# Performance work log

Measured on AMD Instinct MI355X. Metric: run time of the kernel, lower is better.

## Reference

```python
import jax, jax.numpy as jnp
import numpy as np
import math

N_HEAD = 8
D_MODEL = 512
HEAD_SIZE = D_MODEL // N_HEAD
VOCAB = 16384
BLOCK = 512
LN_EPS = 1e-5


def sinusoidal_pe(max_len, dim):
    pos = np.arange(max_len)[:, None].astype(np.float32)
    div = np.exp(np.arange(0, dim, 2).astype(np.float32) * (-math.log(10000.0) / dim))
    pe = np.zeros((max_len, dim), dtype=np.float32)
    pe[:, 0::2] = np.sin(pos * div)
    pe[:, 1::2] = np.cos(pos * div)
    return jnp.asarray(pe)  # (max_len, hs)


def setup_inputs() -> dict:
    key = jax.random.key(0)
    ks = jax.random.split(key, 6)
    b, t = 4, BLOCK
    return {
        "x": jax.random.normal(ks[0], (b, t, 1), dtype=jnp.float32),
        "embedding": jax.random.normal(ks[1], (N_HEAD, VOCAB, HEAD_SIZE), dtype=jnp.float32),
        "enc_w": jax.random.normal(ks[2], (D_MODEL, 1), dtype=jnp.float32) * 0.05,
        "enc_b": jax.random.normal(ks[3], (D_MODEL,), dtype=jnp.float32) * 0.05,
        "ln_w": jnp.ones((HEAD_SIZE,), dtype=jnp.float32),
        "ln_b": jnp.zeros((HEAD_SIZE,), dtype=jnp.float32),
        "dec_w": jax.random.normal(ks[4], (1, D_MODEL), dtype=jnp.float32) * 0.05,
        "dec_b": jax.random.normal(ks[5], (1,), dtype=jnp.float32) * 0.05,
    }


def reference(x, embedding, enc_w, enc_b, ln_w, ln_b, dec_w, dec_b):
    b, t, _ = x.shape
    # encoder: Linear(input_dim -> d_model)
    h = x @ enc_w.T + enc_b                              # (b, t, d_model)
    h = h.reshape(b, t, N_HEAD, HEAD_SIZE).transpose(0, 2, 1, 3)  # (b, nh, t, hs)
    # sinusoidal positional encoding over time, added to head dim
    h = h + sinusoidal_pe(BLOCK, HEAD_SIZE)[:t]
    # LayerNorm over hs
    mu = h.mean(-1, keepdims=True)
    var = ((h - mu) ** 2).mean(-1, keepdims=True)
    h = (h - mu) * jax.lax.rsqrt(var + LN_EPS) * ln_w + ln_b
    # attention over shared per-head codebook
    scores = jnp.einsum('bnth,nvh->bntv', h, embedding) / math.sqrt(D_MODEL)
    probs = jax.nn.softmax(scores, axis=-1)              # (b, nh, t, vocab)
    quant = jnp.einsum('bntv,nvh->bnth', probs, embedding)
    quant = quant.transpose(0, 2, 1, 3).reshape(b, t, D_MODEL)
    # decoder: Linear(d_model -> output_dim)
    return quant @ dec_w.T + dec_b                       # (b, t, 1)
```

## Files before the change

### kernel.cpp

```cpp
#include <hip/hip_runtime.h>
#include <hip/hip_bf16.h>
#include <math.h>

#define NH 8
#define HS 64
#define VOCAB 16384
#define QPH 2048
#define NSLICE 32
#define QSCALE (0.04419417382415922f * 1.4426950408889634f)

typedef __attribute__((ext_vector_type(8))) short bf16x8;
typedef __attribute__((ext_vector_type(4))) float f32x4;

static __device__ __forceinline__ unsigned short f2bf(float f) {
    __hip_bfloat16 h = __float2bfloat16(f);
    unsigned short u;
    __builtin_memcpy(&u, &h, 2);
    return u;
}

static __device__ __forceinline__ float fexp2(float x) {
#if __has_builtin(__builtin_amdgcn_exp2f)
    return __builtin_amdgcn_exp2f(x);
#else
    return __expf(x * 0.6931471805599453f);
#endif
}

__global__ void eprep(const float* __restrict__ emb, const float* __restrict__ dec_w,
                      unsigned short* __restrict__ ebf, float* __restrict__ g) {
    int i4  = blockIdx.x * 256 + threadIdx.x;
    int row = i4 >> 4;
    int c   = i4 & 15;
    int n   = row >> 14;
    f32x4 v = ((const f32x4*)emb)[i4];
    ushort4 u = make_ushort4(f2bf(v.x), f2bf(v.y), f2bf(v.z), f2bf(v.w));
    ((ushort4*)ebf)[i4] = u;
    const float* dw = dec_w + n * 64 + c * 4;
    float p = v.x * dw[0] + v.y * dw[1] + v.z * dw[2] + v.w * dw[3];
    p += __shfl_xor(p, 1); p += __shfl_xor(p, 2);
    p += __shfl_xor(p, 4); p += __shfl_xor(p, 8);
    if (c == 0) g[row] = p;
}

__global__ void qprep(const float* __restrict__ x, const float* __restrict__ enc_w,
                      const float* __restrict__ enc_b, const float* __restrict__ ln_w,
                      const float* __restrict__ ln_b, unsigned short* __restrict__ qbf) {
    int row  = blockIdx.x * 4 + (threadIdx.x >> 6);
    int h    = threadIdx.x & 63;
    int n = row >> 11;
    int q = row & 2047;
    int t = q & 511;
    float xv = x[q];
    int d = n * 64 + h;
    float h2  = (float)(h & ~1);
    float div = __expf(h2 * (-9.210340371976184f / 64.0f));
    float ang = (float)t * div;
    float pe  = (h & 1) ? __cosf(ang) : __sinf(ang);
    float v = xv * enc_w[d] + enc_b[d] + pe;
    float s = v;
    #pragma unroll
    for (int off = 1; off < 64; off <<= 1) s += __shfl_xor(s, off);
    float mu = s * (1.0f / 64.0f);
    float dd = v - mu;
    float s2 = dd * dd;
    #pragma unroll
    for (int off = 1; off < 64; off <<= 1) s2 += __shfl_xor(s2, off);
    float var = s2 * (1.0f / 64.0f);
    float y = dd * rsqrtf(var + 1e-5f) * ln_w[h] + ln_b[h];
    qbf[row * 64 + h] = f2bf(y * QSCALE);
}

__global__ void __launch_bounds__(256, 3)
attn(const unsigned short* __restrict__ qbf, const unsigned short* __restrict__ ebf,
     const float* __restrict__ g, float2* __restrict__ part) {
    int tid  = threadIdx.x;
    int w    = tid >> 6;
    int lane = tid & 63;
    int quad = lane >> 4;
    int l15  = lane & 15;
    int head   = blockIdx.x & 7;
    int vslice = (blockIdx.x >> 3) & 31;
    int qchunk = blockIdx.x >> 8;
    int qbase  = (qchunk * 4 + w) * 128;

    const short* qp = (const short*)qbf + (size_t)(head * QPH + qbase) * HS;
    bf16x8 qf[8][2];
    #pragma unroll
    for (int qt = 0; qt < 8; ++qt) {
        const short* qrow = qp + (qt * 16 + l15) * HS + quad * 8;
        qf[qt][0] = *(const bf16x8*)(qrow);
        qf[qt][1] = *(const bf16x8*)(qrow + 32);
    }

    const short* ep = (const short*)ebf + ((size_t)head * VOCAB + vslice * 512) * HS;
    const float* gp = g + head * VOCAB + vslice * 512;

    float num[8] = {0.f, 0.f, 0.f, 0.f, 0.f, 0.f, 0.f, 0.f};
    float den[8] = {0.f, 0.f, 0.f, 0.f, 0.f, 0.f, 0.f, 0.f};
    const f32x4 z = {0.f, 0.f, 0.f, 0.f};

    #pragma clang loop unroll(disable)
    for (int it = 0; it < 16; ++it) {
        int vb = it * 32;
        const short* e0 = ep + (size_t)(vb + l15) * HS + quad * 8;
        const short* e1 = ep + (size_t)(vb + 16 + l15) * HS + quad * 8;
        bf16x8 a00 = *(const bf16x8*)(e0);
        bf16x8 a01 = *(const bf16x8*)(e0 + 32);
        bf16x8 a10 = *(const bf16x8*)(e1);
        bf16x8 a11 = *(const bf16x8*)(e1 + 32);
        f32x4 gv0 = *(const f32x4*)(gp + vb + quad * 4);
        f32x4 gv1 = *(const f32x4*)(gp + vb + 16 + quad * 4);
        #pragma unroll
        for (int qt = 0; qt < 8; ++qt) {
            f32x4 acc0 = __builtin_amdgcn_mfma_f32_16x16x32_bf16(a00, qf[qt][0], z, 0, 0, 0);
            acc0       = __builtin_amdgcn_mfma_f32_16x16x32_bf16(a01, qf[qt][1], acc0, 0, 0, 0);
            f32x4 acc1 = __builtin_amdgcn_mfma_f32_16x16x32_bf16(a10, qf[qt][0], z, 0, 0, 0);
            acc1       = __builtin_amdgcn_mfma_f32_16x16x32_bf16(a11, qf[qt][1], acc1, 0, 0, 0);
            #pragma unroll
            for (int r = 0; r < 4; ++r) {
                float p0 = fexp2(acc0[r]);
                float p1 = fexp2(acc1[r]);
                den[qt] += p0 + p1;
                num[qt] += p0 * gv0[r] + p1 * gv1[r];
            }
        }
    }

    #pragma unroll
    for (int qt = 0; qt < 8; ++qt) {
        num[qt] += __shfl_xor(num[qt], 16); num[qt] += __shfl_xor(num[qt], 32);
        den[qt] += __shfl_xor(den[qt], 16); den[qt] += __shfl_xor(den[qt], 32);
    }
    #pragma unroll
    for (int j = 0; j < 2; ++j) {
        int qt = quad * 2 + j;
        int qg = qbase + qt * 16 + l15;
        part[((size_t)vslice * NH + head) * QPH + qg] = make_float2(num[qt], den[qt]);
    }
}

__global__ void fin(const float2* __restrict__ part, const float* __restrict__ dec_b,
                    float* __restrict__ out) {
    __shared__ float red[8][32];
    int t  = threadIdx.x;
    int ql = t & 31;
    int n  = t >> 5;
    int q  = blockIdx.x * 32 + ql;
    float nv = 0.f, dv = 0.f;
    #pragma unroll 8
    for (int sl = 0; sl < NSLICE; ++sl) {
        float2 nd = part[((size_t)sl * NH + n) * QPH + q];
        nv += nd.x; dv += nd.y;
    }
    red[n][ql] = nv / dv;
    __syncthreads();
    if (t < 32) {
        float s = dec_b[0];
        #pragma unroll
        for (int m = 0; m < NH; ++m) s += red[m][t];
        out[q] = s;
    }
}

extern "C" void kernel_launch(void* const* d_in, const int* in_sizes, int n_in,
                              void* d_out, int out_size, void* d_ws, size_t ws_size,
                              hipStream_t stream) {
    const float* x     = (const float*)d_in[0];
    const float* emb   = (const float*)d_in[1];
    const float* enc_w = (const float*)d_in[2];
    const float* enc_b = (const float*)d_in[3];
    const float* ln_w  = (const float*)d_in[4];
    const float* ln_b  = (const float*)d_in[5];
    const float* dec_w = (const float*)d_in[6];
    const float* dec_b = (const float*)d_in[7];
    float* out = (float*)d_out;

    char* ws = (char*)d_ws;
    unsigned short* qbf  = (unsigned short*)(ws);
    unsigned short* ebf  = (unsigned short*)(ws + 2097152);
    float*          g    = (float*)(ws + 2097152 + 16777216);
    float2*         part = (float2*)(ws + 2097152 + 16777216 + 524288);

    hipLaunchKernelGGL(eprep, dim3(8192), dim3(256), 0, stream, emb, dec_w, ebf, g);
    hipLaunchKernelGGL(qprep, dim3(4096), dim3(256), 0, stream, x, enc_w, enc_b, ln_w, ln_b, qbf);
    hipLaunchKernelGGL(attn,  dim3(1024), dim3(256), 0, stream, qbf, ebf, g, part);
    hipLaunchKernelGGL(fin,   dim3(64),   dim3(256), 0, stream, part, dec_b, out);
}
```

Before: 149.1 us.

## Stage swizzled codebook tiles into LDS with double-buffered direct loads

The embedding prep kernel now writes the bf16 codebook in a fragment-ordered layout. Each 32-row tile is a contiguous 4 KB block that lands in MFMA operand order. The attention kernel loads these tiles cooperatively into double-buffered LDS with global_load_lds, prefetching the next tile while the current one is used, and it stages the decoder projection vector g in LDS. This removes the redundant per-wave global loads of the same codebook tile, at the cost of a barrier per iteration and 10 KB of LDS. Launch bounds are raised to 4 blocks per SIMD-group to allow more occupancy.

```diff
diff --git a/kernel.cpp b/kernel.cpp
--- a/kernel.cpp
+++ b/kernel.cpp
@@ -27,20 +27,30 @@
 #endif
 }
 
+static __device__ __forceinline__ void stage16(const void* g, void* l) {
+    __builtin_amdgcn_global_load_lds(
+        (const __attribute__((address_space(1))) void*)g,
+        (__attribute__((address_space(3))) void*)l, 16, 0, 0);
+}
+
 __global__ void eprep(const float* __restrict__ emb, const float* __restrict__ dec_w,
                       unsigned short* __restrict__ ebf, float* __restrict__ g) {
     int i4  = blockIdx.x * 256 + threadIdx.x;
     int row = i4 >> 4;
-    int c   = i4 & 15;
+    int c4  = i4 & 15;
     int n   = row >> 14;
-    f32x4 v = ((const f32x4*)emb)[i4];
-    ushort4 u = make_ushort4(f2bf(v.x), f2bf(v.y), f2bf(v.z), f2bf(v.w));
-    ((ushort4*)ebf)[i4] = u;
-    const float* dw = dec_w + n * 64 + c * 4;
-    float p = v.x * dw[0] + v.y * dw[1] + v.z * dw[2] + v.w * dw[3];
+    int v   = row & (VOCAB - 1);
+    f32x4 vv = ((const f32x4*)emb)[i4];
+    ushort4 u = make_ushort4(f2bf(vv.x), f2bf(vv.y), f2bf(vv.z), f2bf(vv.w));
+    int T = v >> 4, r = v & 15;
+    int h = c4 >> 3, q = (c4 >> 1) & 3, jh = c4 & 1;
+    size_t o4 = ((((size_t)(n * 1024 + T) * 2 + h) * 4 + q) * 16 + r) * 2 + jh;
+    ((ushort4*)ebf)[o4] = u;
+    const float* dw = dec_w + n * 64 + c4 * 4;
+    float p = vv.x * dw[0] + vv.y * dw[1] + vv.z * dw[2] + vv.w * dw[3];
     p += __shfl_xor(p, 1); p += __shfl_xor(p, 2);
     p += __shfl_xor(p, 4); p += __shfl_xor(p, 8);
-    if (c == 0) g[row] = p;
+    if (c4 == 0) g[row] = p;
 }
 
 __global__ void qprep(const float* __restrict__ x, const float* __restrict__ enc_w,
@@ -71,9 +81,12 @@
     qbf[row * 64 + h] = f2bf(y * QSCALE);
 }
 
-__global__ void __launch_bounds__(256, 3)
+__global__ void __launch_bounds__(256, 4)
 attn(const unsigned short* __restrict__ qbf, const unsigned short* __restrict__ ebf,
      const float* __restrict__ g, float2* __restrict__ part) {
+    __shared__ __attribute__((aligned(16))) char smem[2 * 4096 + 2048];
+    float* gl = (float*)(smem + 8192);
+
     int tid  = threadIdx.x;
     int w    = tid >> 6;
     int lane = tid & 63;
@@ -84,6 +97,12 @@
     int qchunk = blockIdx.x >> 8;
     int qbase  = (qchunk * 4 + w) * 128;
 
+    const char* esrc = (const char*)ebf + (size_t)(head * 1024 + vslice * 32) * 2048;
+    const float* gp  = g + head * VOCAB + vslice * 512;
+
+    stage16(esrc + tid * 16, smem + w * 1024);
+    ((float2*)gl)[tid] = ((const float2*)gp)[tid];
+
     const short* qp = (const short*)qbf + (size_t)(head * QPH + qbase) * HS;
     bf16x8 qf[8][2];
     #pragma unroll
@@ -93,24 +112,26 @@
         qf[qt][1] = *(const bf16x8*)(qrow + 32);
     }
 
-    const short* ep = (const short*)ebf + ((size_t)head * VOCAB + vslice * 512) * HS;
-    const float* gp = g + head * VOCAB + vslice * 512;
-
     float num[8] = {0.f, 0.f, 0.f, 0.f, 0.f, 0.f, 0.f, 0.f};
     float den[8] = {0.f, 0.f, 0.f, 0.f, 0.f, 0.f, 0.f, 0.f};
     const f32x4 z = {0.f, 0.f, 0.f, 0.f};
 
+    __syncthreads();
+
     #pragma clang loop unroll(disable)
     for (int it = 0; it < 16; ++it) {
-        int vb = it * 32;
-        const short* e0 = ep + (size_t)(vb + l15) * HS + quad * 8;
-        const short* e1 = ep + (size_t)(vb + 16 + l15) * HS + quad * 8;
-        bf16x8 a00 = *(const bf16x8*)(e0);
-        bf16x8 a01 = *(const bf16x8*)(e0 + 32);
-        bf16x8 a10 = *(const bf16x8*)(e1);
-        bf16x8 a11 = *(const bf16x8*)(e1 + 32);
-        f32x4 gv0 = *(const f32x4*)(gp + vb + quad * 4);
-        f32x4 gv1 = *(const f32x4*)(gp + vb + 16 + quad * 4);
+        if (it < 15)
+            stage16(esrc + (it + 1) * 4096 + tid * 16,
+                    smem + ((it + 1) & 1) * 4096 + w * 1024);
+
+        const char* abase = smem + (it & 1) * 4096 + lane * 16;
+        bf16x8 a00 = *(const bf16x8*)(abase);
+        bf16x8 a01 = *(const bf16x8*)(abase + 1024);
+        bf16x8 a10 = *(const bf16x8*)(abase + 2048);
+        bf16x8 a11 = *(const bf16x8*)(abase + 3072);
+        f32x4 gv0 = *(const f32x4*)(gl + it * 32 + quad * 4);
+        f32x4 gv1 = *(const f32x4*)(gl + it * 32 + 16 + quad * 4);
+
         #pragma unroll
         for (int qt = 0; qt < 8; ++qt) {
             f32x4 acc0 = __builtin_amdgcn_mfma_f32_16x16x32_bf16(a00, qf[qt][0], z, 0, 0, 0);
@@ -125,6 +146,7 @@
                 num[qt] += p0 * gv0[r] + p1 * gv1[r];
             }
         }
+        __syncthreads();
     }
 
     #pragma unroll
```

Measured after the change: 155.2 us. +4.1%, slower.
